# Optimization experiments

Measured on AMD Instinct MI355X. Metric: run time of the kernel, lower is better.

## Reference

```python
import jax, jax.numpy as jnp
import numpy as np

N, F, H, E = 8192, 512, 128, 262144
EDGE_REMOVE_RATE = 0.3   # forward arg edge_remove_rate
FEATURE_MASK_RATE = 0.2  # forward arg feature_mask_rate
TEMPERATURE = 0.2        # __init__ temperature


def setup_inputs() -> dict:
    key = jax.random.key(0)
    ks = jax.random.split(key, 8)
    x = jax.random.normal(ks[0], (N, F), jnp.float32)
    row = jax.random.randint(ks[1], (E,), 0, N, dtype=jnp.int32)
    col = jax.random.randint(ks[2], (E,), 0, N, dtype=jnp.int32)
    W_enc = jax.random.normal(ks[3], (F, H), jnp.float32) / np.sqrt(F)
    W_edge = jax.random.normal(ks[4], (2 * H, 1), jnp.float32) / np.sqrt(2 * H)
    b_edge = jnp.zeros((1,), jnp.float32)
    # uniform noise for the RelaxedBernoulli reparameterized sample (one per dense entry)
    noise = jax.random.uniform(ks[5], (N, N), jnp.float32, 1e-6, 1.0 - 1e-6)
    # per-feature uniforms for random_drop_feature's column mask
    mask_u = jax.random.uniform(ks[6], (F,), jnp.float32)
    return dict(x=x, row=row, col=col, W_enc=W_enc, W_edge=W_edge,
                b_edge=b_edge, noise=noise, mask_u=mask_u)


def reference(x, row, col, W_enc, W_edge, b_edge, noise, mask_u):
    # random_drop_feature: zero out columns where uniform < drop_prob
    drop = mask_u < FEATURE_MASK_RATE                      # [F] bool
    feature = jnp.where(drop[None, :], 0.0, x)             # [N, F]

    # encoder(x, sp_adj): 1-layer GCN, sparse A @ (x @ W) via segment_sum over edges
    xw = x @ W_enc                                         # [N, H]
    agg = jax.ops.segment_sum(xw[col], row, num_segments=N)  # [N, H]
    node_emb = jax.nn.relu(agg)

    # fc_edge on concat(node_emb[row], node_emb[col]) == split-weight form
    W1, W2 = W_edge[:H], W_edge[H:]                        # [H,1] each
    edge_logits = (node_emb[row] @ W1 + node_emb[col] @ W2 + b_edge).reshape(-1)  # [E]

    # _norm_to_interval(logits, ub=edge_remove_rate, lb=max(rate-0.5, 0))
    ub = EDGE_REMOVE_RATE
    lb = max(EDGE_REMOVE_RATE - 0.5, 0.0)
    lo = edge_logits.min()
    k = (ub - lb) / (edge_logits.max() - lo)
    edge_probs = lb + k * (edge_logits - lo)               # [E]

    remove_prob = jnp.zeros((N, N), jnp.float32).at[row, col].set(edge_probs)
    sp_dense = jnp.zeros((N, N), jnp.float32).at[row, col].set(1.0)

    # RelaxedBernoulliStraightThrough.rsample():
    #   soft = sigmoid((logit(p) + logistic_noise) / temperature); hard = round(soft)
    eps = 1e-10  # keeps logit(0) finite; sigmoid((log eps)/T) == 0 in fp32
    logit_p = jnp.log(remove_prob + eps) - jnp.log1p(-remove_prob + eps)
    logistic = jnp.log(noise) - jnp.log1p(-noise)
    soft = jax.nn.sigmoid((logit_p + logistic) / TEMPERATURE)
    hard = jnp.round(soft)
    remove_adj = hard + soft - jax.lax.stop_gradient(soft)  # straight-through

    # adj = (1 - remove_adj) * to_dense(sp_adj); aug rate = nnz(adj)/nnz(sp_adj)
    adj = (1.0 - remove_adj) * sp_dense                    # [N, N]
    adj_aug_rate = jnp.sum(adj != 0).astype(jnp.float32) / jnp.sum(sp_dense != 0).astype(jnp.float32)
    return feature, adj, adj_aug_rate
```

## Files before the change

### kernel.cpp

```cpp
#include <hip/hip_runtime.h>
#include <math.h>

constexpr int NND = 8192;
constexpr int FD  = 512;
constexpr int HD  = 128;
constexpr int ED  = 262144;
constexpr long long NF_ = (long long)NND * FD;
constexpr long long NN_ = (long long)NND * NND;

constexpr int SLOT = 72;

constexpr long long Z_K1 = 0;
constexpr long long Z_KD = 6291456;
constexpr long long Z_KE = 8388608;
constexpr long long Z_KF = 14680064;

constexpr int GEMMB = 512;
constexpr int SCAT_BASE = GEMMB;
constexpr int FEAT_BASE = GEMMB + 1024;

typedef float f4nt __attribute__((ext_vector_type(4)));
__device__ __forceinline__ void nt_store(float4* p, float x, float y, float z, float w) {
    f4nt v = {x, y, z, w};
    __builtin_nontemporal_store(v, (f4nt*)p);
}
__device__ __forceinline__ void nt_zero(float4* p) { nt_store(p, 0.f, 0.f, 0.f, 0.f); }


__global__ void k0_init(int* __restrict__ cnt, unsigned* __restrict__ ctrl) {
    int t = blockIdx.x * 256 + threadIdx.x;
    if (t < NND) cnt[t] = 0;
    if (t < 16) ctrl[t] = 0u;
}

__global__ __launch_bounds__(256) void k1_mega(const float* __restrict__ x,
                                               const float* __restrict__ W,
                                               const float* __restrict__ mask_u,
                                               const int* __restrict__ row,
                                               const int* __restrict__ col,
                                               float* __restrict__ out,
                                               float* __restrict__ xw,
                                               int* __restrict__ cnt,
                                               int* __restrict__ slot) {
    __shared__ float Wt[32 * 128];
    __shared__ float Xt[16][32];
    int tid = threadIdx.x;
    if (blockIdx.x < GEMMB) {
        int bid = blockIdx.x;
        int tx = tid & 31, ty = tid >> 5;
        int m0 = bid * 16;
        int r0 = ty * 2, r1 = r0 + 1;
        float a0[4] = {0.f, 0.f, 0.f, 0.f};
        float a1[4] = {0.f, 0.f, 0.f, 0.f};
        for (int kt = 0; kt < FD; kt += 32) {
            const float4* Wq = (const float4*)(W + (long long)kt * HD);
            float4* Wtq = (float4*)Wt;
#pragma unroll
            for (int j = 0; j < 4; ++j)
                Wtq[tid + j * 256] = Wq[tid + j * 256];
            if (tid < 128) {
                int r = tid >> 3, kq = tid & 7;
                ((float4*)&Xt[r][0])[kq] =
                    *(const float4*)(x + (long long)(m0 + r) * FD + kt + kq * 4);
            }
            __syncthreads();
#pragma unroll 8
            for (int kk = 0; kk < 32; ++kk) {
                float s0 = Xt[r0][kk], s1 = Xt[r1][kk];
                const float4 b = *(const float4*)&Wt[kk * 128 + tx * 4];
                a0[0] = fmaf(s0, b.x, a0[0]);
                a0[1] = fmaf(s0, b.y, a0[1]);
                a0[2] = fmaf(s0, b.z, a0[2]);
                a0[3] = fmaf(s0, b.w, a0[3]);
                a1[0] = fmaf(s1, b.x, a1[0]);
                a1[1] = fmaf(s1, b.y, a1[1]);
                a1[2] = fmaf(s1, b.z, a1[2]);
                a1[3] = fmaf(s1, b.w, a1[3]);
            }
            __syncthreads();
        }
        *(float4*)(xw + (long long)(m0 + r0) * HD + tx * 4) =
            make_float4(a0[0], a0[1], a0[2], a0[3]);
        *(float4*)(xw + (long long)(m0 + r1) * HD + tx * 4) =
            make_float4(a1[0], a1[1], a1[2], a1[3]);
    } else if (blockIdx.x < FEAT_BASE) {
        int e = (blockIdx.x - SCAT_BASE) * 256 + tid;
        int r = row[e];
        int pos = atomicAdd(&cnt[r], 1);
        slot[r * SLOT + pos] = (e << 13) | col[e];
        float4* zq = (float4*)(out + NF_);
#pragma unroll
        for (int j = 0; j < 8; ++j)
            nt_zero(&zq[Z_KD + e + (long long)j * ED]);
    } else {
        int fid = (blockIdx.x - FEAT_BASE) * 256 + tid;
        int c4 = (fid & 127) * 4;
        float kx = (mask_u[c4 + 0] < 0.2f) ? 0.f : 1.f;
        float ky = (mask_u[c4 + 1] < 0.2f) ? 0.f : 1.f;
        float kz = (mask_u[c4 + 2] < 0.2f) ? 0.f : 1.f;
        float kw = (mask_u[c4 + 3] < 0.2f) ? 0.f : 1.f;
        const float4* xq = (const float4*)x;
        float4* oq = (float4*)out;
#pragma unroll
        for (int j = 0; j < 4; ++j) {
            long long q = fid + (long long)j * 262144;
            float4 xv = xq[q];
            nt_store(&oq[q], xv.x * kx, xv.y * ky, xv.z * kz, xv.w * kw);
        }
        float4* zq = (float4*)(out + NF_);
#pragma unroll
        for (int j = 0; j < 24; ++j)
            nt_zero(&zq[Z_K1 + fid + (long long)j * 262144]);
    }
}

__global__ __launch_bounds__(128) void kE_spmm_uv(const float* __restrict__ xw,
                                                  const int* __restrict__ cnt,
                                                  const int* __restrict__ slot,
                                                  const float* __restrict__ Wedge,
                                                  float* __restrict__ u,
                                                  float* __restrict__ v,
                                                  float4* __restrict__ zq) {
    int i = blockIdx.x, t = threadIdx.x;
    int n = cnt[i];
    const int* sp = slot + i * SLOT;
    float acc = 0.f;
    int j = 0;
    for (; j + 4 <= n; j += 4) {
        int c0 = sp[j] & 8191, c1 = sp[j + 1] & 8191;
        int c2 = sp[j + 2] & 8191, c3 = sp[j + 3] & 8191;
        float v0 = xw[(long long)c0 * HD + t];
        float v1 = xw[(long long)c1 * HD + t];
        float v2 = xw[(long long)c2 * HD + t];
        float v3 = xw[(long long)c3 * HD + t];
        acc += v0; acc += v1; acc += v2; acc += v3;
    }
    for (; j < n; ++j) acc += xw[(long long)(sp[j] & 8191) * HD + t];
    acc = fmaxf(acc, 0.f);

    float up = acc * Wedge[t];
    float vp = acc * Wedge[HD + t];
#pragma unroll
    for (int off = 32; off > 0; off >>= 1) {
        up += __shfl_down(up, off);
        vp += __shfl_down(vp, off);
    }
    __shared__ float su[2], sv[2];
    int wid = t >> 6;
    if ((t & 63) == 0) { su[wid] = up; sv[wid] = vp; }
    __syncthreads();
    if (t == 0) { u[i] = su[0] + su[1]; v[i] = sv[0] + sv[1]; }

    long long ft = (long long)i * 128 + t;
#pragma unroll
    for (int jj = 0; jj < 6; ++jj)
        nt_zero(&zq[Z_KE + ft + (long long)jj * 1048576]);
}

__global__ __launch_bounds__(256) void kF_minmax(const int* __restrict__ row,
                                                 const int* __restrict__ col,
                                                 const float* __restrict__ u,
                                                 const float* __restrict__ v,
                                                 const float* __restrict__ b_edge,
                                                 float* __restrict__ pmn,
                                                 float* __restrict__ pmx,
                                                 unsigned* __restrict__ ctrl,
                                                 float4* __restrict__ zq) {
    int gid = blockIdx.x * 256 + threadIdx.x;
    float el = u[row[gid]] + v[col[gid]] + b_edge[0];

#pragma unroll
    for (int j = 0; j < 8; ++j)
        nt_zero(&zq[Z_KF + gid + (long long)j * ED]);

    float mn = el, mx = el;
#pragma unroll
    for (int off = 32; off > 0; off >>= 1) {
        mn = fminf(mn, __shfl_xor(mn, off));
        mx = fmaxf(mx, __shfl_xor(mx, off));
    }
    __shared__ float smn[4], smx[4];
    __shared__ unsigned tkt;
    int w = threadIdx.x >> 6;
    if ((threadIdx.x & 63) == 0) { smn[w] = mn; smx[w] = mx; }
    __syncthreads();
    if (threadIdx.x == 0) {
        pmn[blockIdx.x] = fminf(fminf(smn[0], smn[1]), fminf(smn[2], smn[3]));
        pmx[blockIdx.x] = fmaxf(fmaxf(smx[0], smx[1]), fmaxf(smx[2], smx[3]));
        __threadfence();
        tkt = atomicAdd(&ctrl[4], 1u);
    }
    __syncthreads();
    if (tkt == gridDim.x - 1) {
        __threadfence();
        int t = threadIdx.x;
        float4 a = ((const float4*)pmn)[t];
        float4 b = ((const float4*)pmx)[t];
        float m2 = fminf(fminf(a.x, a.y), fminf(a.z, a.w));
        float x2 = fmaxf(fmaxf(b.x, b.y), fmaxf(b.z, b.w));
#pragma unroll
        for (int off = 32; off > 0; off >>= 1) {
            m2 = fminf(m2, __shfl_xor(m2, off));
            x2 = fmaxf(x2, __shfl_xor(x2, off));
        }
        __shared__ float rmn[4], rmx[4];
        if ((t & 63) == 0) { rmn[t >> 6] = m2; rmx[t >> 6] = x2; }
        __syncthreads();
        if (t == 0) {
            float* flh = (float*)&ctrl[8];
            flh[0] = fminf(fminf(rmn[0], rmn[1]), fminf(rmn[2], rmn[3]));
            flh[1] = fmaxf(fmaxf(rmx[0], rmx[1]), fmaxf(rmx[2], rmx[3]));
        }
    }
}

__global__ __launch_bounds__(256) void kZ_patch(const int* __restrict__ cnt,
                                                const int* __restrict__ slot,
                                                const float* __restrict__ u,
                                                const float* __restrict__ v,
                                                const float* __restrict__ b_edge,
                                                const float* __restrict__ noise,
                                                float* __restrict__ adj,
                                                int* __restrict__ pcu,
                                                int* __restrict__ pcz,
                                                unsigned* __restrict__ ctrl,
                                                float* __restrict__ rate) {
    const int tid = threadIdx.x;
    const int b = blockIdx.x;
    __shared__ int skey[8 * SLOT];
    __shared__ int scnt[8];
    __shared__ float su_[8];
    if (tid < 8) {
        scnt[tid] = cnt[b * 8 + tid];
        su_[tid] = u[b * 8 + tid];
    }
    __syncthreads();
#pragma unroll
    for (int rl = 0; rl < 8; ++rl) {
        int n = scnt[rl];
        for (int i = tid; i < n; i += 256)
            skey[rl * SLOT + i] = slot[(b * 8 + rl) * SLOT + i];
    }
    __syncthreads();

    const float* flh = (const float*)&ctrl[8];
    const float lo = flh[0];
    const float hi = flh[1];
    const float kk = 0.3f / (hi - lo);
    const float be = b_edge[0];

    int uniq = 0, nzc = 0;
#pragma unroll
    for (int rl = 0; rl < 8; ++rl) {
        int n = scnt[rl];
        const int* kp = skey + rl * SLOT;
        for (int i = tid; i < n; i += 256) {
            int key = kp[i];
            int c = key & 8191;
            bool win = true;
            for (int j = 0; j < n; ++j) {
                int kj = kp[j];
                if ((kj & 8191) == c && kj > key) { win = false; break; }
            }
            if (!win) continue;
            ++uniq;
            float el = su_[rl] + v[c] + be;
            float pr = kk * (el - lo);
            float lp = logf(pr + 1e-10f) - log1pf(1e-10f - pr);
            float nz = noise[(long long)(b * 8 + rl) * NND + c];
            float lg = logf(nz) - log1pf(-nz);
            if ((lp + lg) <= 0.f) {
                ++nzc;
                adj[(long long)(b * 8 + rl) * NND + c] = 1.0f;
            }
        }
    }

#pragma unroll
    for (int off = 32; off > 0; off >>= 1) {
        uniq += __shfl_down(uniq, off);
        nzc  += __shfl_down(nzc, off);
    }
    __shared__ int scu[4], scz[4];
    __shared__ unsigned tkt;
    int wd = tid >> 6;
    if ((tid & 63) == 0) { scu[wd] = uniq; scz[wd] = nzc; }
    __syncthreads();
    if (tid == 0) {
        pcu[b] = scu[0] + scu[1] + scu[2] + scu[3];
        pcz[b] = scz[0] + scz[1] + scz[2] + scz[3];
        __threadfence();
        tkt = atomicAdd(&ctrl[5], 1u);
    }
    __syncthreads();
    if (tkt == gridDim.x - 1) {
        __threadfence();
        int t = tid;
        int4 a = ((const int4*)pcu)[t];
        int4 bq = ((const int4*)pcz)[t];
        int cu = a.x + a.y + a.z + a.w;
        int cz = bq.x + bq.y + bq.z + bq.w;
#pragma unroll
        for (int off = 32; off > 0; off >>= 1) {
            cu += __shfl_down(cu, off);
            cz += __shfl_down(cz, off);
        }
        __shared__ int rcu[4], rcz[4];
        if ((t & 63) == 0) { rcu[t >> 6] = cu; rcz[t >> 6] = cz; }
        __syncthreads();
        if (t == 0)
            rate[0] = (float)(rcz[0] + rcz[1] + rcz[2] + rcz[3]) /
                      (float)(rcu[0] + rcu[1] + rcu[2] + rcu[3]);
    }
}

extern "C" void kernel_launch(void* const* d_in, const int* in_sizes, int n_in,
                              void* d_out, int out_size, void* d_ws, size_t ws_size,
                              hipStream_t stream) {
    const float* x     = (const float*)d_in[0];
    const int*   row   = (const int*)d_in[1];
    const int*   col   = (const int*)d_in[2];
    const float* Wenc  = (const float*)d_in[3];
    const float* Wedge = (const float*)d_in[4];
    const float* bedge = (const float*)d_in[5];
    const float* noise = (const float*)d_in[6];
    const float* masku = (const float*)d_in[7];
    float* out = (float*)d_out;

    char* ws = (char*)d_ws;
    float* xw   = (float*)(ws);
    int*   slot = (int*)  (ws + 4194304);
    float* u    = (float*)(ws + 6553600);
    float* v    = (float*)(ws + 6586368);
    int*   cnt  = (int*)  (ws + 6619136);
    int*   pcu  = (int*)  (ws + 6651904);
    int*   pcz  = (int*)  (ws + 6656000);
    float* pmn  = (float*)(ws + 6660096);
    float* pmx  = (float*)(ws + 6664192);
    unsigned* ctrl = (unsigned*)(ws + 6668288);

    float4* zq  = (float4*)(out + NF_);
    float*  adj = out + NF_;
    float* rate = out + NF_ + NN_;

    k0_init<<<32, 256, 0, stream>>>(cnt, ctrl);
    k1_mega<<<GEMMB + 1024 + 1024, 256, 0, stream>>>(x, Wenc, masku, row, col,
                                                     out, xw, cnt, slot);
    kE_spmm_uv<<<8192, 128, 0, stream>>>(xw, cnt, slot, Wedge, u, v, zq);
    kF_minmax<<<1024, 256, 0, stream>>>(row, col, u, v, bedge, pmn, pmx, ctrl, zq);
    kZ_patch<<<1024, 256, 0, stream>>>(cnt, slot, u, v, bedge, noise, adj,
                                       pcu, pcz, ctrl, rate);
}
```

Baseline: 192.5 us.

## Retile encoder GEMM per wavefront, read W directly from global/L2

Restructures the x@W_enc GEMM inside the fused first kernel. Each block now covers 32 rows, split as 8 rows per 64-lane wavefront, with every lane computing a 2x8 output tile. The W tile is no longer staged in shared memory and is read straight from global memory, relying on the cache since W is only 256KB. X is stored transposed in shared memory, so the GEMM grid halves and shared-memory use drops, in exchange for more global/L2 traffic on W.

```diff
diff --git a/kernel.cpp b/kernel.cpp
--- a/kernel.cpp
+++ b/kernel.cpp
@@ -15,7 +15,7 @@
 constexpr long long Z_KE = 8388608;
 constexpr long long Z_KF = 14680064;
 
-constexpr int GEMMB = 512;
+constexpr int GEMMB = 256;
 constexpr int SCAT_BASE = GEMMB;
 constexpr int FEAT_BASE = GEMMB + 1024;
 
@@ -42,47 +42,47 @@
                                                float* __restrict__ xw,
                                                int* __restrict__ cnt,
                                                int* __restrict__ slot) {
-    __shared__ float Wt[32 * 128];
-    __shared__ float Xt[16][32];
+    __shared__ float Xt[4][32][8];
     int tid = threadIdx.x;
     if (blockIdx.x < GEMMB) {
         int bid = blockIdx.x;
-        int tx = tid & 31, ty = tid >> 5;
-        int m0 = bid * 16;
-        int r0 = ty * 2, r1 = r0 + 1;
-        float a0[4] = {0.f, 0.f, 0.f, 0.f};
-        float a1[4] = {0.f, 0.f, 0.f, 0.f};
+        int wv = tid >> 6;
+        int lane = tid & 63;
+        int tx = lane & 15;
+        int ty = lane >> 4;
+        int m0w = bid * 32 + wv * 8;
+        int rs = lane & 7;
+        int kq = lane >> 3;
+        float a0[8] = {0.f, 0.f, 0.f, 0.f, 0.f, 0.f, 0.f, 0.f};
+        float a1[8] = {0.f, 0.f, 0.f, 0.f, 0.f, 0.f, 0.f, 0.f};
         for (int kt = 0; kt < FD; kt += 32) {
-            const float4* Wq = (const float4*)(W + (long long)kt * HD);
-            float4* Wtq = (float4*)Wt;
-#pragma unroll
-            for (int j = 0; j < 4; ++j)
-                Wtq[tid + j * 256] = Wq[tid + j * 256];
-            if (tid < 128) {
-                int r = tid >> 3, kq = tid & 7;
-                ((float4*)&Xt[r][0])[kq] =
-                    *(const float4*)(x + (long long)(m0 + r) * FD + kt + kq * 4);
-            }
+            float4 xv = *(const float4*)(x + (long long)(m0w + rs) * FD + kt + kq * 4);
+            Xt[wv][kq * 4 + 0][rs] = xv.x;
+            Xt[wv][kq * 4 + 1][rs] = xv.y;
+            Xt[wv][kq * 4 + 2][rs] = xv.z;
+            Xt[wv][kq * 4 + 3][rs] = xv.w;
             __syncthreads();
 #pragma unroll 8
             for (int kk = 0; kk < 32; ++kk) {
-                float s0 = Xt[r0][kk], s1 = Xt[r1][kk];
-                const float4 b = *(const float4*)&Wt[kk * 128 + tx * 4];
-                a0[0] = fmaf(s0, b.x, a0[0]);
-                a0[1] = fmaf(s0, b.y, a0[1]);
-                a0[2] = fmaf(s0, b.z, a0[2]);
-                a0[3] = fmaf(s0, b.w, a0[3]);
-                a1[0] = fmaf(s1, b.x, a1[0]);
-                a1[1] = fmaf(s1, b.y, a1[1]);
-                a1[2] = fmaf(s1, b.z, a1[2]);
-                a1[3] = fmaf(s1, b.w, a1[3]);
+                const float* wr = W + (long long)(kt + kk) * HD + tx * 8;
+                float4 b0 = *(const float4*)wr;
+                float4 b1 = *(const float4*)(wr + 4);
+                float2 xr = *(const float2*)&Xt[wv][kk][ty * 2];
+                float bs[8] = {b0.x, b0.y, b0.z, b0.w, b1.x, b1.y, b1.z, b1.w};
+#pragma unroll
+                for (int ci = 0; ci < 8; ++ci) {
+                    a0[ci] = fmaf(xr.x, bs[ci], a0[ci]);
+                    a1[ci] = fmaf(xr.y, bs[ci], a1[ci]);
+                }
             }
             __syncthreads();
         }
-        *(float4*)(xw + (long long)(m0 + r0) * HD + tx * 4) =
-            make_float4(a0[0], a0[1], a0[2], a0[3]);
-        *(float4*)(xw + (long long)(m0 + r1) * HD + tx * 4) =
-            make_float4(a1[0], a1[1], a1[2], a1[3]);
+        float* o0 = xw + (long long)(m0w + ty * 2) * HD + tx * 8;
+        float* o1 = o0 + HD;
+        *(float4*)o0 = make_float4(a0[0], a0[1], a0[2], a0[3]);
+        *(float4*)(o0 + 4) = make_float4(a0[4], a0[5], a0[6], a0[7]);
+        *(float4*)o1 = make_float4(a1[0], a1[1], a1[2], a1[3]);
+        *(float4*)(o1 + 4) = make_float4(a1[4], a1[5], a1[6], a1[7]);
     } else if (blockIdx.x < FEAT_BASE) {
         int e = (blockIdx.x - SCAT_BASE) * 256 + tid;
         int r = row[e];
```

Result: slower. 232.0 us (+20.5%).
